# Performance work log

Measured on AMD Instinct MI355X. Metric: run time of the kernel, lower is better.

Reference implementation:

```python
import jax, jax.numpy as jnp
import numpy as np

N_NODES = 50000


def gcn_conv(x, edge_index, W, b, n_nodes):
    # PyG GCNConv: h = D^{-1/2} (A + I) D^{-1/2} (x @ W) + b
    loops = jnp.arange(n_nodes, dtype=edge_index.dtype)
    src = jnp.concatenate([edge_index[0], loops])
    dst = jnp.concatenate([edge_index[1], loops])
    deg = jax.ops.segment_sum(jnp.ones_like(dst, dtype=x.dtype), dst,
                              num_segments=n_nodes)
    dinv = jnp.where(deg > 0, jax.lax.rsqrt(deg), 0.0)
    norm = dinv[src] * dinv[dst]                      # [E+N]
    h = x @ W                                          # [N, out]
    msg = h[src] * norm[:, None]                       # gather + scale
    out = jax.ops.segment_sum(msg, dst, num_segments=n_nodes)
    return out + b


def setup_inputs() -> dict:
    key = jax.random.key(0)
    ks = jax.random.split(key, 8)
    in_c, hid_c, out_c = 256, 128, 64
    x = jax.random.normal(ks[0], (N_NODES, in_c), dtype=jnp.float32)
    edge_index = jax.random.randint(ks[1], (2, 800000), 0, N_NODES, dtype=jnp.int64)
    pos_edge_index = jax.random.randint(ks[2], (2, 200000), 0, N_NODES, dtype=jnp.int64)
    neg_edge_index = jax.random.randint(ks[3], (2, 200000), 0, N_NES if False else N_NODES, dtype=jnp.int64)
    W1 = jax.random.normal(ks[4], (in_c, hid_c), dtype=jnp.float32) / np.sqrt(in_c)
    b1 = jnp.zeros((hid_c,), dtype=jnp.float32)
    W2 = jax.random.normal(ks[5], (hid_c, out_c), dtype=jnp.float32) / np.sqrt(hid_c)
    b2 = jnp.zeros((out_c,), dtype=jnp.float32)
    return {"x": x, "edge_index": edge_index, "pos_edge_index": pos_edge_index,
            "neg_edge_index": neg_edge_index, "W1": W1, "b1": b1, "W2": W2, "b2": b2}


def reference(x, edge_index, pos_edge_index, neg_edge_index, W1, b1, W2, b2):
    n = x.shape[0]
    h = jax.nn.relu(gcn_conv(x, edge_index, W1, b1, n))
    z = gcn_conv(h, edge_index, W2, b2, n)             # [N, out_c]
    ei = jnp.concatenate([pos_edge_index, neg_edge_index], axis=-1)
    logits = jnp.sum(z[ei[0]] * z[ei[1]], axis=-1)     # [E_pos + E_neg]
    return logits
```

## Files before the change

kernel.cpp:

```cpp
#include <hip/hip_runtime.h>
#include <stdint.h>

constexpr int N_NODES = 50000;
constexpr int E_EDGES = 800000;
constexpr int E_PAIR  = 200000;
constexpr int C_IN    = 256;
constexpr int C_HID   = 128;
constexpr int C_OUT   = 64;
constexpr int SLOT    = 64;

constexpr int NBUCK = 196;
constexpr int BCAP  = 4608;
constexpr int CHUNK = 2048;
constexpr int PREPB = 32;
constexpr int BINAB = (E_EDGES + CHUNK - 1) / CHUNK;
constexpr int GEMM1_BLOCKS = (N_NODES + 63) / 64;

typedef __attribute__((ext_vector_type(8))) _Float16 f16x8;
typedef __attribute__((ext_vector_type(2))) _Float16 f16x2;
typedef __attribute__((ext_vector_type(4))) float f32x4;

__device__ inline uint16_t f2h_bits(float v) {
    union { _Float16 h; uint16_t u; } c; c.h = (_Float16)v;
    return c.u;
}
__device__ inline uint32_t pack2h(float a, float b) {
    return (uint32_t)f2h_bits(a) | ((uint32_t)f2h_bits(b) << 16);
}
__device__ inline void acc_h8(float* a, uint4 v) {
    union { uint4 u; _Float16 h[8]; } c; c.u = v;
#pragma unroll
    for (int i = 0; i < 8; ++i) a[i] += (float)c.h[i];
}
__device__ inline void acc_h8s(float* a, uint4 v, float s) {
    union { uint4 u; _Float16 h[8]; } c; c.u = v;
#pragma unroll
    for (int i = 0; i < 8; ++i) a[i] += (float)c.h[i] * s;
}
__device__ inline float dot_h8(uint4 a, uint4 b) {
    union { uint4 u; f16x2 h[4]; } ca, cb; ca.u = a; cb.u = b;
    float v = 0.f;
#pragma unroll
    for (int i = 0; i < 4; ++i) {
#if __has_builtin(__builtin_amdgcn_fdot2)
        v = __builtin_amdgcn_fdot2(ca.h[i], cb.h[i], v, false);
#else
        v += (float)ca.h[i][0] * (float)cb.h[i][0]
           + (float)ca.h[i][1] * (float)cb.h[i][1];
#endif
    }
    return v;
}

template<int N>
__device__ inline int wswz_idx(int k, int n) {
    int c = k >> 5, kq = (k >> 3) & 3, kk = k & 7, ct = n >> 4, nn = n & 15;
    return (((c * (N / 16) + ct) * 4 + kq) * 16 + nn) * 8 + kk;
}

__global__ __launch_bounds__(256) void prep_binA_kernel(
        const float* __restrict__ W1, const float* __restrict__ W2,
        uint16_t* __restrict__ s1, uint16_t* __restrict__ s2,
        const int* __restrict__ src, const int* __restrict__ dst,
        int* __restrict__ gcur, uint32_t* __restrict__ ebuf) {
    __shared__ int cnt[NBUCK], loc[NBUCK], lim[NBUCK], abase[NBUCK], wcur[NBUCK];
    __shared__ int tot;
    __shared__ uint32_t stag[CHUNK];
    __shared__ uint8_t  bof[CHUNK];

    const int t = threadIdx.x;

    if (blockIdx.x < PREPB) {
        for (int id = blockIdx.x * 256 + t;
             id < C_IN * C_HID + C_HID * C_OUT; id += PREPB * 256) {
            if (id < C_IN * C_HID) {
                int idx = wswz_idx<C_HID>(id / C_HID, id & (C_HID - 1));
                s1[idx] = f2h_bits(W1[id]);
            } else {
                int id2 = id - C_IN * C_HID;
                int idx = wswz_idx<C_OUT>(id2 / C_OUT, id2 & (C_OUT - 1));
                s2[idx] = f2h_bits(W2[id2]);
            }
        }
        return;
    }

    const int e0 = (blockIdx.x - PREPB) * CHUNK;
    const int n  = min(CHUNK, E_EDGES - e0);

    for (int b = t; b < NBUCK; b += 256) cnt[b] = 0;
    if (t == 0) tot = 0;
    __syncthreads();

    uint32_t pk[CHUNK / 256]; int bk[CHUNK / 256];
    int ne = 0;
    for (int j = t; j < n; j += 256) {
        int d = dst[e0 + j], s = src[e0 + j];
        int b = d >> 8;
        pk[ne] = ((uint32_t)(d & 255) << 16) | (uint32_t)s;
        bk[ne] = b;
        atomicAdd(&cnt[b], 1);
        ++ne;
    }
    __syncthreads();
    for (int b = t; b < NBUCK; b += 256)
        loc[b] = atomicAdd(&tot, cnt[b]);
    __syncthreads();
    for (int b = t; b < NBUCK; b += 256) {
        int base = atomicAdd(&gcur[b], cnt[b]);
        int room = BCAP - base; if (room < 0) room = 0;
        lim[b]   = loc[b] + room;
        abase[b] = b * BCAP + base - loc[b];
        wcur[b]  = loc[b];
    }
    __syncthreads();
#pragma unroll
    for (int i = 0; i < CHUNK / 256; ++i) {
        if (i < ne) {
            int p = atomicAdd(&wcur[bk[i]], 1);
            stag[p] = pk[i];
            bof[p]  = (uint8_t)bk[i];
        }
    }
    __syncthreads();
    for (int j = t; j < n; j += 256) {
        int b = bof[j];
        if (j < lim[b]) ebuf[abase[b] + j] = stag[j];
    }
}

__global__ __launch_bounds__(256, 3) void build_gemm_kernel(
        const int* __restrict__ gcur, const uint32_t* __restrict__ ebuf,
        uint16_t* __restrict__ col2, int* __restrict__ degc,
        float* __restrict__ dinv,
        const float* __restrict__ A, const uint16_t* __restrict__ Bswz,
        uint16_t* __restrict__ out) {
    constexpr int K = C_IN, N = C_HID;
    constexpr int BM = 64, BK = 32;
    constexpr int CT   = N / 32;
    constexpr int NSUB = N / 16;
    constexpr int ABYTES = BM * BK * 2;
    constexpr int BBYTES = NSUB * 1024;
    __shared__ char sm[ABYTES + BBYTES];

    const int t = threadIdx.x;

    if (blockIdx.x < NBUCK) {
        int* cur = (int*)sm;
        const int b = blockIdx.x;
        cur[t] = 0;
        __syncthreads();

        int cn = gcur[b]; if (cn > BCAP) cn = BCAP;
        const uint32_t* eb = ebuf + (size_t)b * BCAP;
        const size_t nbase = (size_t)b << 8;

        int j = t;
        for (; j + 3 * 256 < cn; j += 4 * 256) {
            uint32_t v0 = eb[j], v1 = eb[j + 256], v2 = eb[j + 512], v3 = eb[j + 768];
            int p0 = atomicAdd(&cur[v0 >> 16], 1);
            int p1 = atomicAdd(&cur[v1 >> 16], 1);
            int p2 = atomicAdd(&cur[v2 >> 16], 1);
            int p3 = atomicAdd(&cur[v3 >> 16], 1);
            if (p0 < SLOT) col2[((nbase + (v0 >> 16)) << 6) + p0] = (uint16_t)(v0 & 0xffff);
            if (p1 < SLOT) col2[((nbase + (v1 >> 16)) << 6) + p1] = (uint16_t)(v1 & 0xffff);
            if (p2 < SLOT) col2[((nbase + (v2 >> 16)) << 6) + p2] = (uint16_t)(v2 & 0xffff);
            if (p3 < SLOT) col2[((nbase + (v3 >> 16)) << 6) + p3] = (uint16_t)(v3 & 0xffff);
        }
        for (; j < cn; j += 256) {
            uint32_t v = eb[j];
            int p = atomicAdd(&cur[v >> 16], 1);
            if (p < SLOT) col2[((nbase + (v >> 16)) << 6) + p] = (uint16_t)(v & 0xffff);
        }
        __syncthreads();
        int node = (int)nbase + t;
        if (node < N_NODES) {
            int dg = cur[t];
            degc[node] = dg;
            dinv[node] = rsqrtf((float)dg + 1.0f);
        }
        return;
    }

    char* As = sm;
    char* Bs = sm + ABYTES;

    const int lane = t & 63;
    const int w    = t >> 6;
    const int wrow = w & 1, wcol = w >> 1;
    const int m0   = (blockIdx.x - NBUCK) * BM;
    const int M    = N_NODES;

    const int sr = t >> 2, skq = t & 3;
    int arow = m0 + sr; if (arow > M - 1) arow = M - 1;
    const float* aptr = A + (size_t)arow * K + skq * 8;
    const int aslot = ((sr >> 4) * 64 + skq * 16 + (sr & 15)) * 16;

    f32x4 acc[2][CT];
#pragma unroll
    for (int rt = 0; rt < 2; ++rt)
#pragma unroll
        for (int ct = 0; ct < CT; ++ct) {
            f32x4 z = {0.f, 0.f, 0.f, 0.f};
            acc[rt][ct] = z;
        }

    const uint4* gh = (const uint4*)Bswz;

    constexpr int NCH = K / BK;
#pragma unroll 1
    for (int c = 0; c < NCH; ++c) {
        float4 v0 = *(const float4*)(aptr + c * BK);
        float4 v1 = *(const float4*)(aptr + c * BK + 4);
        uint4 bh0, bh1;
        {
            const uint4* ch = gh + (size_t)c * (BBYTES / 16);
            bh0 = ch[t];
            bh1 = ch[t + 256];
        }
        __syncthreads();
        {
            float e[8] = {v0.x, v0.y, v0.z, v0.w, v1.x, v1.y, v1.z, v1.w};
            uint32_t hp[4];
#pragma unroll
            for (int j = 0; j < 4; ++j)
                hp[j] = pack2h(e[2 * j], e[2 * j + 1]);
            *(uint4*)(As + aslot) = make_uint4(hp[0], hp[1], hp[2], hp[3]);
        }
        *(uint4*)(Bs + t * 16) = bh0;
        *(uint4*)(Bs + (t + 256) * 16) = bh1;
        __syncthreads();
        f16x8 Ah[2];
#pragma unroll
        for (int rt = 0; rt < 2; ++rt) {
            int st = wrow * 2 + rt;
            Ah[rt] = *(const f16x8*)(As + st * 1024 + lane * 16);
        }
#pragma unroll
        for (int ct = 0; ct < CT; ++ct) {
            int cg = wcol * CT + ct;
            f16x8 Bh = *(const f16x8*)(Bs + cg * 1024 + lane * 16);
#pragma unroll
            for (int rt = 0; rt < 2; ++rt)
                acc[rt][ct] = __builtin_amdgcn_mfma_f32_16x16x32_f16(Ah[rt], Bh, acc[rt][ct], 0, 0, 0);
        }
    }

#pragma unroll
    for (int rt = 0; rt < 2; ++rt) {
        int rowbase = m0 + wrow * 32 + rt * 16 + (lane >> 4) * 4;
#pragma unroll
        for (int ct = 0; ct < CT; ++ct) {
            int n = (wcol * CT + ct) * 16 + (lane & 15);
#pragma unroll
            for (int r = 0; r < 4; ++r) {
                int m = rowbase + r;
                if (m < M) out[(size_t)m * N + n] = f2h_bits(acc[rt][ct][r]);
            }
        }
    }
}

__global__ __launch_bounds__(512) void gather_gemm_kernel(
        const uint16_t* __restrict__ col2, const int* __restrict__ degc,
        const uint16_t* __restrict__ h0u, const float* __restrict__ dinv,
        const float* __restrict__ bias, const uint16_t* __restrict__ B2swz,
        uint16_t* __restrict__ z0s) {
    __shared__ uint4 hlds[256];
    const int t    = threadIdx.x;
    const int lane = t & 63;
    const int w    = t >> 6;
    const int g32  = lane >> 5;
    const int q    = lane & 31;
    const int team = q >> 4;
    const int l    = q & 15;
    const int node_loc = w * 2 + g32;
    const int node = blockIdx.x * 16 + node_loc;

    int dg = degc[node]; if (dg > SLOT) dg = SLOT;
    const float dn = dinv[node];
    const uint4* hs4 = (const uint4*)h0u;
    float a0[8], a1[8];
#pragma unroll
    for (int i = 0; i < 8; ++i) { a0[i] = 0.f; a1[i] = 0.f; }
    if (team == 0) {
        uint4 self = hs4[(size_t)node * 16 + l];
        acc_h8s(a0, self, dn);
    }
    const int base = node * SLOT;
    const int wb   = (lane & 32) | (team << 4);

    for (int c = 0; c * 16 < dg; ++c) {
        int off = c * 16 + (team << 3);
        int cnt = dg - off; if (cnt < 0) cnt = 0; if (cnt > 8) cnt = 8;
        int cv = (l < cnt) ? (int)col2[base + off + l] : 0;
        int j = 0;
        for (; j + 8 <= cnt; j += 8) {
            int s0 = __shfl(cv, wb + j,     64);
            int s1 = __shfl(cv, wb + j + 1, 64);
            int s2 = __shfl(cv, wb + j + 2, 64);
            int s3 = __shfl(cv, wb + j + 3, 64);
            int s4 = __shfl(cv, wb + j + 4, 64);
            int s5 = __shfl(cv, wb + j + 5, 64);
            int s6 = __shfl(cv, wb + j + 6, 64);
            int s7 = __shfl(cv, wb + j + 7, 64);
            uint4 v0 = hs4[(size_t)s0 * 16 + l];
            uint4 v1 = hs4[(size_t)s1 * 16 + l];
            uint4 v2 = hs4[(size_t)s2 * 16 + l];
            uint4 v3 = hs4[(size_t)s3 * 16 + l];
            uint4 v4 = hs4[(size_t)s4 * 16 + l];
            uint4 v5 = hs4[(size_t)s5 * 16 + l];
            uint4 v6 = hs4[(size_t)s6 * 16 + l];
            uint4 v7 = hs4[(size_t)s7 * 16 + l];
            float d0 = dinv[s0], d1 = dinv[s1], d2 = dinv[s2], d3 = dinv[s3];
            float d4 = dinv[s4], d5 = dinv[s5], d6 = dinv[s6], d7 = dinv[s7];
            acc_h8s(a0, v0, d0); acc_h8s(a1, v1, d1);
            acc_h8s(a0, v2, d2); acc_h8s(a1, v3, d3);
            acc_h8s(a0, v4, d4); acc_h8s(a1, v5, d5);
            acc_h8s(a0, v6, d6); acc_h8s(a1, v7, d7);
        }
        for (; j + 4 <= cnt; j += 4) {
            int s0 = __shfl(cv, wb + j,     64);
            int s1 = __shfl(cv, wb + j + 1, 64);
            int s2 = __shfl(cv, wb + j + 2, 64);
            int s3 = __shfl(cv, wb + j + 3, 64);
            uint4 v0 = hs4[(size_t)s0 * 16 + l];
            uint4 v1 = hs4[(size_t)s1 * 16 + l];
            uint4 v2 = hs4[(size_t)s2 * 16 + l];
            uint4 v3 = hs4[(size_t)s3 * 16 + l];
            float d0 = dinv[s0], d1 = dinv[s1], d2 = dinv[s2], d3 = dinv[s3];
            acc_h8s(a0, v0, d0); acc_h8s(a1, v1, d1);
            acc_h8s(a0, v2, d2); acc_h8s(a1, v3, d3);
        }
        for (; j < cnt; ++j) {
            int s = __shfl(cv, wb + j, 64);
            uint4 v = hs4[(size_t)s * 16 + l];
            acc_h8s(a0, v, dinv[s]);
        }
    }
    {
        float av[8];
#pragma unroll
        for (int i = 0; i < 8; ++i) {
            av[i] = a0[i] + a1[i];
            av[i] += __shfl_xor(av[i], 16, 64);
        }
        float4 bb0 = ((const float4*)bias)[2 * l];
        float4 bb1 = ((const float4*)bias)[2 * l + 1];
        float o[8];
        o[0] = fmaxf(av[0] * dn + bb0.x, 0.f);
        o[1] = fmaxf(av[1] * dn + bb0.y, 0.f);
        o[2] = fmaxf(av[2] * dn + bb0.z, 0.f);
        o[3] = fmaxf(av[3] * dn + bb0.w, 0.f);
        o[4] = fmaxf(av[4] * dn + bb1.x, 0.f);
        o[5] = fmaxf(av[5] * dn + bb1.y, 0.f);
        o[6] = fmaxf(av[6] * dn + bb1.z, 0.f);
        o[7] = fmaxf(av[7] * dn + bb1.w, 0.f);
        if (team == 0)
            hlds[l * 16 + node_loc] = make_uint4(
                pack2h(o[0], o[1]), pack2h(o[2], o[3]),
                pack2h(o[4], o[5]), pack2h(o[6], o[7]));
    }
    __syncthreads();

    if (t < 256) {
        f32x4 acc = {0.f, 0.f, 0.f, 0.f};
        const char* hb = (const char*)hlds;
#pragma unroll
        for (int c = 0; c < 4; ++c) {
            f16x8 Af = *(const f16x8*)(hb + c * 1024 + lane * 16);
            f16x8 Bh = *(const f16x8*)(B2swz + (c * 4 + w) * 512 + lane * 8);
            acc = __builtin_amdgcn_mfma_f32_16x16x32_f16(Af, Bh, acc, 0, 0, 0);
        }
        const int colg = w * 16 + (lane & 15);
        const int rowb = blockIdx.x * 16 + (lane >> 4) * 4;
#pragma unroll
        for (int r = 0; r < 4; ++r) {
            int m = rowb + r;
            z0s[(size_t)m * C_OUT + colg] = f2h_bits(acc[r] * dinv[m]);
        }
    }
}

template<int F, bool RELU>
__global__ __launch_bounds__(256) void gather_kernel(
        const uint16_t* __restrict__ col2, const int* __restrict__ degc,
        const uint16_t* __restrict__ hs, const float* __restrict__ dinv,
        const float* __restrict__ bias, uint16_t* __restrict__ out) {
    constexpr int LPN = F / 8;
    const int lane = threadIdx.x & 63;
    const int q    = lane & 15;
    const int team = q >> 3;
    const int l    = q & 7;
    const int node = blockIdx.x * 16 + (threadIdx.x >> 6) * 4 + (lane >> 4);
    if (node >= N_NODES) return;

    int dg = degc[node]; if (dg > SLOT) dg = SLOT;
    const uint4* hs4 = (const uint4*)hs;

    float a0[8], a1[8];
#pragma unroll
    for (int i = 0; i < 8; ++i) { a0[i] = 0.f; a1[i] = 0.f; }
    if (team == 0) {
        uint4 self = hs4[(size_t)node * LPN + l];
        acc_h8(a0, self);
    }
    const int base = node * SLOT;
    const int wb   = (lane & 48) | (team << 3);

    for (int c = 0; c * 16 < dg; ++c) {
        int off = c * 16 + (team << 3);
        int cnt = dg - off; if (cnt < 0) cnt = 0; if (cnt > 8) cnt = 8;
        int cv = (l < cnt) ? (int)col2[base + off + l] : 0;
        int j = 0;
        for (; j + 8 <= cnt; j += 8) {
            int s0 = __shfl(cv, wb + j,     64);
            int s1 = __shfl(cv, wb + j + 1, 64);
            int s2 = __shfl(cv, wb + j + 2, 64);
            int s3 = __shfl(cv, wb + j + 3, 64);
            int s4 = __shfl(cv, wb + j + 4, 64);
            int s5 = __shfl(cv, wb + j + 5, 64);
            int s6 = __shfl(cv, wb + j + 6, 64);
            int s7 = __shfl(cv, wb + j + 7, 64);
            uint4 v0 = hs4[(size_t)s0 * LPN + l];
            uint4 v1 = hs4[(size_t)s1 * LPN + l];
            uint4 v2 = hs4[(size_t)s2 * LPN + l];
            uint4 v3 = hs4[(size_t)s3 * LPN + l];
            uint4 v4 = hs4[(size_t)s4 * LPN + l];
            uint4 v5 = hs4[(size_t)s5 * LPN + l];
            uint4 v6 = hs4[(size_t)s6 * LPN + l];
            uint4 v7 = hs4[(size_t)s7 * LPN + l];
            acc_h8(a0, v0); acc_h8(a1, v1);
            acc_h8(a0, v2); acc_h8(a1, v3);
            acc_h8(a0, v4); acc_h8(a1, v5);
            acc_h8(a0, v6); acc_h8(a1, v7);
        }
        for (; j + 4 <= cnt; j += 4) {
            int s0 = __shfl(cv, wb + j,     64);
            int s1 = __shfl(cv, wb + j + 1, 64);
            int s2 = __shfl(cv, wb + j + 2, 64);
            int s3 = __shfl(cv, wb + j + 3, 64);
            uint4 v0 = hs4[(size_t)s0 * LPN + l];
            uint4 v1 = hs4[(size_t)s1 * LPN + l];
            uint4 v2 = hs4[(size_t)s2 * LPN + l];
            uint4 v3 = hs4[(size_t)s3 * LPN + l];
            acc_h8(a0, v0); acc_h8(a1, v1);
            acc_h8(a0, v2); acc_h8(a1, v3);
        }
        for (; j < cnt; ++j) {
            int s = __shfl(cv, wb + j, 64);
            uint4 v = hs4[(size_t)s * LPN + l];
            acc_h8(a0, v);
        }
    }

    const float dn = dinv[node];
    float av[8];
#pragma unroll
    for (int i = 0; i < 8; ++i) {
        av[i] = a0[i] + a1[i];
        av[i] += __shfl_xor(av[i], 8, 64);
    }
    float4 bb0 = ((const float4*)bias)[2 * l];
    float4 bb1 = ((const float4*)bias)[2 * l + 1];
    float o[8];
    o[0] = av[0] * dn + bb0.x;
    o[1] = av[1] * dn + bb0.y;
    o[2] = av[2] * dn + bb0.z;
    o[3] = av[3] * dn + bb0.w;
    o[4] = av[4] * dn + bb1.x;
    o[5] = av[5] * dn + bb1.y;
    o[6] = av[6] * dn + bb1.z;
    o[7] = av[7] * dn + bb1.w;
    if (RELU) {
#pragma unroll
        for (int i = 0; i < 8; ++i) o[i] = fmaxf(o[i], 0.f);
    }
    if (team == 0) {
        uint4 res = make_uint4(pack2h(o[0], o[1]), pack2h(o[2], o[3]),
                               pack2h(o[4], o[5]), pack2h(o[6], o[7]));
        ((uint4*)out)[(size_t)node * LPN + l] = res;
    }
}

__global__ __launch_bounds__(256) void logits_kernel(
        const int* __restrict__ pos, const int* __restrict__ neg,
        const uint16_t* __restrict__ z, float* __restrict__ out) {
    const int t = threadIdx.x;
    const int l = t & 7;
    const int g = (blockIdx.x * 256 + t) >> 3;
    const int e0 = 2 * g;
    if (e0 >= 2 * E_PAIR) return;
    int s0, d0, s1, d1;
    if (e0 < E_PAIR) { s0 = pos[e0];          d0 = pos[E_PAIR + e0]; }
    else             { s0 = neg[e0 - E_PAIR]; d0 = neg[e0];          }
    int e1 = e0 + 1;
    if (e1 < E_PAIR) { s1 = pos[e1];          d1 = pos[E_PAIR + e1]; }
    else             { s1 = neg[e1 - E_PAIR]; d1 = neg[e1];          }
    const uint4* z4 = (const uint4*)z;
    uint4 ua0 = z4[(size_t)s0 * 8 + l];
    uint4 ub0 = z4[(size_t)d0 * 8 + l];
    uint4 ua1 = z4[(size_t)s1 * 8 + l];
    uint4 ub1 = z4[(size_t)d1 * 8 + l];
    float v0 = dot_h8(ua0, ub0);
    float v1 = dot_h8(ua1, ub1);
    v0 += __shfl_xor(v0, 1, 64); v1 += __shfl_xor(v1, 1, 64);
    v0 += __shfl_xor(v0, 2, 64); v1 += __shfl_xor(v1, 2, 64);
    v0 += __shfl_xor(v0, 4, 64); v1 += __shfl_xor(v1, 4, 64);
    if (l == 0) { out[e0] = v0; out[e1] = v1; }
}

extern "C" void kernel_launch(void* const* d_in, const int* in_sizes, int n_in,
                              void* d_out, int out_size, void* d_ws, size_t ws_size,
                              hipStream_t stream) {
    const float* x   = (const float*)d_in[0];
    const int*   ei  = (const int*)d_in[1];
    const int*   pos = (const int*)d_in[2];
    const int*   neg = (const int*)d_in[3];
    const float* W1  = (const float*)d_in[4];
    const float* b1  = (const float*)d_in[5];
    const float* W2  = (const float*)d_in[6];
    const float* b2  = (const float*)d_in[7];
    float* out = (float*)d_out;

    const int* src = ei;
    const int* dst = ei + E_EDGES;

    char* ws = (char*)d_ws;
    int*      degc  = (int*)ws;
    float*    dinv  = (float*)(ws + 200704);
    uint16_t* col2  = (uint16_t*)(ws + 401408);
    int*      gcur  = (int*)(ws + 6801408);
    uint16_t* B1swz = (uint16_t*)(ws + 6802432);
    uint16_t* B2swz = (uint16_t*)(ws + 6933504);
    uint16_t* h0u   = (uint16_t*)(ws + 6966272);
    uint16_t* z0s   = (uint16_t*)(ws + 32566272);
    uint16_t* zbuf  = (uint16_t*)(ws + 38966272);
    uint32_t* ebuf  = (uint32_t*)(ws + 45366272);

    hipMemsetAsync(gcur, 0, NBUCK * sizeof(int), stream);

    prep_binA_kernel<<<PREPB + BINAB, 256, 0, stream>>>(
        W1, W2, B1swz, B2swz, src, dst, gcur, ebuf);

    build_gemm_kernel<<<NBUCK + GEMM1_BLOCKS, 256, 0, stream>>>(
        gcur, ebuf, col2, degc, dinv, x, B1swz, h0u);

    gather_gemm_kernel<<<N_NODES / 16, 512, 0, stream>>>(
        col2, degc, h0u, dinv, b1, B2swz, z0s);

    gather_kernel<C_OUT, false><<<(N_NODES + 15) / 16, 256, 0, stream>>>(
        col2, degc, z0s, dinv, b2, zbuf);

    logits_kernel<<<(E_PAIR * 8 + 255) / 256, 256, 0, stream>>>(pos, neg, zbuf, out);
}
```

Baseline: 202.5 us.

## Drop two-team edge split; one lane group per node with packed index loads

Both gather kernels previously split each node's neighbor list across two teams of lanes and combined the partial sums with a cross-lane shuffle reduction. Now a single group of lanes (LPN lanes) handles each node, so twice as many nodes are processed per wavefront. The gather_gemm kernel shrinks to 256-thread blocks, and the second gather launches half as many blocks. Neighbor indices are read as packed 32-bit pairs, which halves the index loads and shuffles. The cost is less memory-level parallelism per node, since each node's edges are now walked sequentially by one lane group, and there is more per-node latency for high-degree nodes.

```diff
diff --git a/kernel.cpp b/kernel.cpp
--- a/kernel.cpp
+++ b/kernel.cpp
@@ -261,7 +261,7 @@
     }
 }
 
-__global__ __launch_bounds__(512) void gather_gemm_kernel(
+__global__ __launch_bounds__(256) void gather_gemm_kernel(
         const uint16_t* __restrict__ col2, const int* __restrict__ degc,
         const uint16_t* __restrict__ h0u, const float* __restrict__ dinv,
         const float* __restrict__ bias, const uint16_t* __restrict__ B2swz,
@@ -270,11 +270,9 @@
     const int t    = threadIdx.x;
     const int lane = t & 63;
     const int w    = t >> 6;
-    const int g32  = lane >> 5;
-    const int q    = lane & 31;
-    const int team = q >> 4;
-    const int l    = q & 15;
-    const int node_loc = w * 2 + g32;
+    const int sub  = lane >> 4;
+    const int l    = lane & 15;
+    const int node_loc = w * 4 + sub;
     const int node = blockIdx.x * 16 + node_loc;
 
     int dg = degc[node]; if (dg > SLOT) dg = SLOT;
@@ -283,27 +281,27 @@
     float a0[8], a1[8];
 #pragma unroll
     for (int i = 0; i < 8; ++i) { a0[i] = 0.f; a1[i] = 0.f; }
-    if (team == 0) {
+    {
         uint4 self = hs4[(size_t)node * 16 + l];
         acc_h8s(a0, self, dn);
     }
-    const int base = node * SLOT;
-    const int wb   = (lane & 32) | (team << 4);
+    const uint32_t* cp = (const uint32_t*)col2;
+    const int pbase = node * (SLOT / 2);
+    const int sb    = sub * 16;
 
     for (int c = 0; c * 16 < dg; ++c) {
-        int off = c * 16 + (team << 3);
-        int cnt = dg - off; if (cnt < 0) cnt = 0; if (cnt > 8) cnt = 8;
-        int cv = (l < cnt) ? (int)col2[base + off + l] : 0;
+        int cnt = dg - c * 16; if (cnt > 16) cnt = 16;
+        uint32_t cv = (2 * l < cnt) ? cp[pbase + c * 8 + l] : 0u;
         int j = 0;
         for (; j + 8 <= cnt; j += 8) {
-            int s0 = __shfl(cv, wb + j,     64);
-            int s1 = __shfl(cv, wb + j + 1, 64);
-            int s2 = __shfl(cv, wb + j + 2, 64);
-            int s3 = __shfl(cv, wb + j + 3, 64);
-            int s4 = __shfl(cv, wb + j + 4, 64);
-            int s5 = __shfl(cv, wb + j + 5, 64);
-            int s6 = __shfl(cv, wb + j + 6, 64);
-            int s7 = __shfl(cv, wb + j + 7, 64);
+            uint32_t p0 = (uint32_t)__shfl((int)cv, sb + (j >> 1),     64);
+            uint32_t p1 = (uint32_t)__shfl((int)cv, sb + (j >> 1) + 1, 64);
+            uint32_t p2 = (uint32_t)__shfl((int)cv, sb + (j >> 1) + 2, 64);
+            uint32_t p3 = (uint32_t)__shfl((int)cv, sb + (j >> 1) + 3, 64);
+            int s0 = p0 & 0xffff, s1 = p0 >> 16;
+            int s2 = p1 & 0xffff, s3 = p1 >> 16;
+            int s4 = p2 & 0xffff, s5 = p2 >> 16;
+            int s6 = p3 & 0xffff, s7 = p3 >> 16;
             uint4 v0 = hs4[(size_t)s0 * 16 + l];
             uint4 v1 = hs4[(size_t)s1 * 16 + l];
             uint4 v2 = hs4[(size_t)s2 * 16 + l];
@@ -320,10 +318,10 @@
             acc_h8s(a0, v6, d6); acc_h8s(a1, v7, d7);
         }
         for (; j + 4 <= cnt; j += 4) {
-            int s0 = __shfl(cv, wb + j,     64);
-            int s1 = __shfl(cv, wb + j + 1, 64);
-            int s2 = __shfl(cv, wb + j + 2, 64);
-            int s3 = __shfl(cv, wb + j + 3, 64);
+            uint32_t p0 = (uint32_t)__shfl((int)cv, sb + (j >> 1),     64);
+            uint32_t p1 = (uint32_t)__shfl((int)cv, sb + (j >> 1) + 1, 64);
+            int s0 = p0 & 0xffff, s1 = p0 >> 16;
+            int s2 = p1 & 0xffff, s3 = p1 >> 16;
             uint4 v0 = hs4[(size_t)s0 * 16 + l];
             uint4 v1 = hs4[(size_t)s1 * 16 + l];
             uint4 v2 = hs4[(size_t)s2 * 16 + l];
@@ -333,52 +331,44 @@
             acc_h8s(a0, v2, d2); acc_h8s(a1, v3, d3);
         }
         for (; j < cnt; ++j) {
-            int s = __shfl(cv, wb + j, 64);
+            uint32_t p = (uint32_t)__shfl((int)cv, sb + (j >> 1), 64);
+            int s = (j & 1) ? (int)(p >> 16) : (int)(p & 0xffff);
             uint4 v = hs4[(size_t)s * 16 + l];
             acc_h8s(a0, v, dinv[s]);
         }
     }
     {
-        float av[8];
-#pragma unroll
-        for (int i = 0; i < 8; ++i) {
-            av[i] = a0[i] + a1[i];
-            av[i] += __shfl_xor(av[i], 16, 64);
-        }
         float4 bb0 = ((const float4*)bias)[2 * l];
         float4 bb1 = ((const float4*)bias)[2 * l + 1];
         float o[8];
-        o[0] = fmaxf(av[0] * dn + bb0.x, 0.f);
-        o[1] = fmaxf(av[1] * dn + bb0.y, 0.f);
-        o[2] = fmaxf(av[2] * dn + bb0.z, 0.f);
-        o[3] = fmaxf(av[3] * dn + bb0.w, 0.f);
-        o[4] = fmaxf(av[4] * dn + bb1.x, 0.f);
-        o[5] = fmaxf(av[5] * dn + bb1.y, 0.f);
-        o[6] = fmaxf(av[6] * dn + bb1.z, 0.f);
-        o[7] = fmaxf(av[7] * dn + bb1.w, 0.f);
-        if (team == 0)
-            hlds[l * 16 + node_loc] = make_uint4(
-                pack2h(o[0], o[1]), pack2h(o[2], o[3]),
-                pack2h(o[4], o[5]), pack2h(o[6], o[7]));
+        o[0] = fmaxf((a0[0] + a1[0]) * dn + bb0.x, 0.f);
+        o[1] = fmaxf((a0[1] + a1[1]) * dn + bb0.y, 0.f);
+        o[2] = fmaxf((a0[2] + a1[2]) * dn + bb0.z, 0.f);
+        o[3] = fmaxf((a0[3] + a1[3]) * dn + bb0.w, 0.f);
+        o[4] = fmaxf((a0[4] + a1[4]) * dn + bb1.x, 0.f);
+        o[5] = fmaxf((a0[5] + a1[5]) * dn + bb1.y, 0.f);
+        o[6] = fmaxf((a0[6] + a1[6]) * dn + bb1.z, 0.f);
+        o[7] = fmaxf((a0[7] + a1[7]) * dn + bb1.w, 0.f);
+        hlds[l * 16 + node_loc] = make_uint4(
+            pack2h(o[0], o[1]), pack2h(o[2], o[3]),
+            pack2h(o[4], o[5]), pack2h(o[6], o[7]));
     }
     __syncthreads();
 
-    if (t < 256) {
-        f32x4 acc = {0.f, 0.f, 0.f, 0.f};
-        const char* hb = (const char*)hlds;
-#pragma unroll
-        for (int c = 0; c < 4; ++c) {
-            f16x8 Af = *(const f16x8*)(hb + c * 1024 + lane * 16);
-            f16x8 Bh = *(const f16x8*)(B2swz + (c * 4 + w) * 512 + lane * 8);
-            acc = __builtin_amdgcn_mfma_f32_16x16x32_f16(Af, Bh, acc, 0, 0, 0);
-        }
-        const int colg = w * 16 + (lane & 15);
-        const int rowb = blockIdx.x * 16 + (lane >> 4) * 4;
-#pragma unroll
-        for (int r = 0; r < 4; ++r) {
-            int m = rowb + r;
-            z0s[(size_t)m * C_OUT + colg] = f2h_bits(acc[r] * dinv[m]);
-        }
+    f32x4 acc = {0.f, 0.f, 0.f, 0.f};
+    const char* hb = (const char*)hlds;
+#pragma unroll
+    for (int c = 0; c < 4; ++c) {
+        f16x8 Af = *(const f16x8*)(hb + c * 1024 + lane * 16);
+        f16x8 Bh = *(const f16x8*)(B2swz + (c * 4 + w) * 512 + lane * 8);
+        acc = __builtin_amdgcn_mfma_f32_16x16x32_f16(Af, Bh, acc, 0, 0, 0);
+    }
+    const int colg = w * 16 + (lane & 15);
+    const int rowb = blockIdx.x * 16 + (lane >> 4) * 4;
+#pragma unroll
+    for (int r = 0; r < 4; ++r) {
+        int m = rowb + r;
+        z0s[(size_t)m * C_OUT + colg] = f2h_bits(acc[r] * dinv[m]);
     }
 }
 
@@ -388,11 +378,11 @@
         const uint16_t* __restrict__ hs, const float* __restrict__ dinv,
         const float* __restrict__ bias, uint16_t* __restrict__ out) {
     constexpr int LPN = F / 8;
+    constexpr int NPW = 64 / LPN;
     const int lane = threadIdx.x & 63;
-    const int q    = lane & 15;
-    const int team = q >> 3;
-    const int l    = q & 7;
-    const int node = blockIdx.x * 16 + (threadIdx.x >> 6) * 4 + (lane >> 4);
+    const int sub  = lane / LPN;
+    const int l    = lane % LPN;
+    const int node = blockIdx.x * (4 * NPW) + (threadIdx.x >> 6) * NPW + sub;
     if (node >= N_NODES) return;
 
     int dg = degc[node]; if (dg > SLOT) dg = SLOT;
@@ -401,27 +391,27 @@
     float a0[8], a1[8];
 #pragma unroll
     for (int i = 0; i < 8; ++i) { a0[i] = 0.f; a1[i] = 0.f; }
-    if (team == 0) {
+    {
         uint4 self = hs4[(size_t)node * LPN + l];
         acc_h8(a0, self);
     }
-    const int base = node * SLOT;
-    const int wb   = (lane & 48) | (team << 3);
-
-    for (int c = 0; c * 16 < dg; ++c) {
-        int off = c * 16 + (team << 3);
-        int cnt = dg - off; if (cnt < 0) cnt = 0; if (cnt > 8) cnt = 8;
-        int cv = (l < cnt) ? (int)col2[base + off + l] : 0;
+    const uint32_t* cp = (const uint32_t*)col2;
+    const int pbase = node * (SLOT / 2);
+    const int sb    = sub * LPN;
+
+    for (int c = 0; c * LPN < dg; ++c) {
+        int cnt = dg - c * LPN; if (cnt > LPN) cnt = LPN;
+        uint32_t cv = (2 * l < cnt) ? cp[pbase + c * (LPN / 2) + l] : 0u;
         int j = 0;
         for (; j + 8 <= cnt; j += 8) {
-            int s0 = __shfl(cv, wb + j,     64);
-            int s1 = __shfl(cv, wb + j + 1, 64);
-            int s2 = __shfl(cv, wb + j + 2, 64);
-            int s3 = __shfl(cv, wb + j + 3, 64);
-            int s4 = __shfl(cv, wb + j + 4, 64);
-            int s5 = __shfl(cv, wb + j + 5, 64);
-            int s6 = __shfl(cv, wb + j + 6, 64);
-            int s7 = __shfl(cv, wb + j + 7, 64);
+            uint32_t p0 = (uint32_t)__shfl((int)cv, sb + (j >> 1),     64);
+            uint32_t p1 = (uint32_t)__shfl((int)cv, sb + (j >> 1) + 1, 64);
+            uint32_t p2 = (uint32_t)__shfl((int)cv, sb + (j >> 1) + 2, 64);
+            uint32_t p3 = (uint32_t)__shfl((int)cv, sb + (j >> 1) + 3, 64);
+            int s0 = p0 & 0xffff, s1 = p0 >> 16;
+            int s2 = p1 & 0xffff, s3 = p1 >> 16;
+            int s4 = p2 & 0xffff, s5 = p2 >> 16;
+            int s6 = p3 & 0xffff, s7 = p3 >> 16;
             uint4 v0 = hs4[(size_t)s0 * LPN + l];
             uint4 v1 = hs4[(size_t)s1 * LPN + l];
             uint4 v2 = hs4[(size_t)s2 * LPN + l];
@@ -436,10 +426,10 @@
             acc_h8(a0, v6); acc_h8(a1, v7);
         }
         for (; j + 4 <= cnt; j += 4) {
-            int s0 = __shfl(cv, wb + j,     64);
-            int s1 = __shfl(cv, wb + j + 1, 64);
-            int s2 = __shfl(cv, wb + j + 2, 64);
-            int s3 = __shfl(cv, wb + j + 3, 64);
+            uint32_t p0 = (uint32_t)__shfl((int)cv, sb + (j >> 1),     64);
+            uint32_t p1 = (uint32_t)__shfl((int)cv, sb + (j >> 1) + 1, 64);
+            int s0 = p0 & 0xffff, s1 = p0 >> 16;
+            int s2 = p1 & 0xffff, s3 = p1 >> 16;
             uint4 v0 = hs4[(size_t)s0 * LPN + l];
             uint4 v1 = hs4[(size_t)s1 * LPN + l];
             uint4 v2 = hs4[(size_t)s2 * LPN + l];
@@ -448,39 +438,32 @@
             acc_h8(a0, v2); acc_h8(a1, v3);
         }
         for (; j < cnt; ++j) {
-            int s = __shfl(cv, wb + j, 64);
+            uint32_t p = (uint32_t)__shfl((int)cv, sb + (j >> 1), 64);
+            int s = (j & 1) ? (int)(p >> 16) : (int)(p & 0xffff);
             uint4 v = hs4[(size_t)s * LPN + l];
             acc_h8(a0, v);
         }
     }
 
     const float dn = dinv[node];
-    float av[8];
-#pragma unroll
-    for (int i = 0; i < 8; ++i) {
-        av[i] = a0[i] + a1[i];
-        av[i] += __shfl_xor(av[i], 8, 64);
-    }
     float4 bb0 = ((const float4*)bias)[2 * l];
     float4 bb1 = ((const float4*)bias)[2 * l + 1];
     float o[8];
-    o[0] = av[0] * dn + bb0.x;
-    o[1] = av[1] * dn + bb0.y;
-    o[2] = av[2] * dn + bb0.z;
-    o[3] = av[3] * dn + bb0.w;
-    o[4] = av[4] * dn + bb1.x;
-    o[5] = av[5] * dn + bb1.y;
-    o[6] = av[6] * dn + bb1.z;
-    o[7] = av[7] * dn + bb1.w;
+    o[0] = (a0[0] + a1[0]) * dn + bb0.x;
+    o[1] = (a0[1] + a1[1]) * dn + bb0.y;
+    o[2] = (a0[2] + a1[2]) * dn + bb0.z;
+    o[3] = (a0[3] + a1[3]) * dn + bb0.w;
+    o[4] = (a0[4] + a1[4]) * dn + bb1.x;
+    o[5] = (a0[5] + a1[5]) * dn + bb1.y;
+    o[6] = (a0[6] + a1[6]) * dn + bb1.z;
+    o[7] = (a0[7] + a1[7]) * dn + bb1.w;
     if (RELU) {
 #pragma unroll
         for (int i = 0; i < 8; ++i) o[i] = fmaxf(o[i], 0.f);
     }
-    if (team == 0) {
-        uint4 res = make_uint4(pack2h(o[0], o[1]), pack2h(o[2], o[3]),
-                               pack2h(o[4], o[5]), pack2h(o[6], o[7]));
-        ((uint4*)out)[(size_t)node * LPN + l] = res;
-    }
+    uint4 res = make_uint4(pack2h(o[0], o[1]), pack2h(o[2], o[3]),
+                           pack2h(o[4], o[5]), pack2h(o[6], o[7]));
+    ((uint4*)out)[(size_t)node * LPN + l] = res;
 }
 
 __global__ __launch_bounds__(256) void logits_kernel(
@@ -546,10 +529,10 @@
     build_gemm_kernel<<<NBUCK + GEMM1_BLOCKS, 256, 0, stream>>>(
         gcur, ebuf, col2, degc, dinv, x, B1swz, h0u);
 
-    gather_gemm_kernel<<<N_NODES / 16, 512, 0, stream>>>(
+    gather_gemm_kernel<<<N_NODES / 16, 256, 0, stream>>>(
         col2, degc, h0u, dinv, b1, B2swz, z0s);
 
-    gather_kernel<C_OUT, false><<<(N_NODES + 15) / 16, 256, 0, stream>>>(
+    gather_kernel<C_OUT, false><<<(N_NODES + 31) / 32, 256, 0, stream>>>(
         col2, degc, z0s, dinv, b2, zbuf);
 
     logits_kernel<<<(E_PAIR * 8 + 255) / 256, 256, 0, stream>>>(pos, neg, zbuf, out);
```

New measurement: 198.0 us. 2.2% less time.
